# Performance work log

Measured on AMD Instinct MI355X. Metric: run time of the kernel, lower is better.

## Reference

```python
import jax, jax.numpy as jnp
import numpy as np

TOP_K = 2


def setup_inputs() -> dict:
    key = jax.random.key(0)
    k1, k2, k3, k4, k5 = jax.random.split(key, 5)
    B, S, H, F, E = 4, 2048, 1024, 4096, 8
    scale = 1.0 / np.sqrt(H)
    return {
        "hidden_states": jax.random.normal(k1, (B, S, H), dtype=jnp.float32),
        "gate_w": jax.random.normal(k2, (E, H), dtype=jnp.float32) * scale,
        "w1": jax.random.normal(k3, (E, F, H), dtype=jnp.float32) * scale,
        "w3": jax.random.normal(k4, (E, F, H), dtype=jnp.float32) * scale,
        "w2": jax.random.normal(k5, (E, H, F), dtype=jnp.float32) * (1.0 / np.sqrt(F)),
    }


def reference(hidden_states, gate_w, w1, w3, w2):
    B, S, H = hidden_states.shape
    E = gate_w.shape[0]
    x = hidden_states.reshape(-1, H)                    # [T, H], T = B*S

    router_logits = x @ gate_w.T                        # [T, E]
    probs = jax.nn.softmax(router_logits.astype(jnp.float32), axis=-1)
    top_w, top_i = jax.lax.top_k(probs, TOP_K)          # [T, k]
    top_w = top_w / jnp.sum(top_w, axis=-1, keepdims=True)
    top_w = top_w.astype(x.dtype)

    # combine weight of each expert for each token: [E, T]
    one_hot = jax.nn.one_hot(top_i, E, dtype=x.dtype)   # [T, k, E]
    comb = jnp.einsum("tke,tk->et", one_hot, top_w)

    # loop over experts via scan; tokens not routed to expert e have comb==0,
    # which matches the gather/FFN/scatter-combine of the original exactly.
    def body(acc, wts):
        w1e, w3e, w2e, ce = wts
        h = jax.nn.silu(x @ w1e.T) * (x @ w3e.T)        # [T, F]
        return acc + (h @ w2e.T) * ce[:, None], None

    out0 = jnp.zeros_like(x)
    out, _ = jax.lax.scan(body, out0, (w1, w3, w2, comb))
    return out.reshape(B, S, H), router_logits
```

## Files before the change

kernel.cpp:

```cpp
#include <hip/hip_runtime.h>
#include <hip/hip_bf16.h>

#define T_TOK 8192
#define HDIM  1024
#define FDIM  4096
#define NEXP  8
#define CVT_BLKS 2048
#define RT_MAX 24

typedef __attribute__((ext_vector_type(8))) short short8;
typedef __attribute__((ext_vector_type(4))) float f32x4;
typedef unsigned short u16;
typedef unsigned int   u32;

#define XB_OFF    0ull
#define W1B_OFF   (XB_OFF   + 16777216ull)
#define W3B_OFF   (W1B_OFF  + 67108864ull)
#define W2B_OFF   (W3B_OFF  + 67108864ull)
#define HBUF_OFF  (W2B_OFF  + 67108864ull)
#define CNT_OFF   (HBUF_OFF + 134217728ull)
#define TLIST_OFF (CNT_OFF  + 128ull)
#define WLIST_OFF (TLIST_OFF + 262144ull)
#define WS_NEED   (WLIST_OFF + 262144ull)

__device__ __forceinline__ u16 f2bf(float f) {
  u32 u = __float_as_uint(f);
  return (u16)((u + 0x7fffu + ((u >> 16) & 1u)) >> 16);
}
__device__ __forceinline__ float bf2f(u16 v) {
  return __uint_as_float((u32)v << 16);
}

__device__ __forceinline__ void gl_lds16(const void* g, void* l) {
  __builtin_amdgcn_global_load_lds(
      (const __attribute__((address_space(1))) void*)g,
      (__attribute__((address_space(3))) void*)l, 16, 0, 0);
}

__global__ __launch_bounds__(256) void prep_kernel(
    const float* __restrict__ x, const float* __restrict__ gw,
    const float* __restrict__ s0, const float* __restrict__ s1,
    u16* __restrict__ d0, u16* __restrict__ d1,
    float* __restrict__ logits, u16* __restrict__ xb,
    int* __restrict__ counts, int* __restrict__ tlist,
    float* __restrict__ wt1, float* __restrict__ wt2,
    int* __restrict__ slot1, int* __restrict__ slot2) {
  if (blockIdx.x < 8192) {
    const int n8 = NEXP * FDIM * HDIM / 8;
    const int total = 2 * n8;
    const int stride = 8192 * 256;
    for (int i = blockIdx.x * 256 + threadIdx.x; i < total; i += stride) {
      int seg = i >> 22;
      int j = i & (n8 - 1);
      const float* s = seg == 0 ? s0 : s1;
      u16* d = seg == 0 ? d0 : d1;
      float4 v0 = ((const float4*)s)[j * 2];
      float4 v1 = ((const float4*)s)[j * 2 + 1];
      uint4 o;
      o.x = (u32)f2bf(v0.x) | ((u32)f2bf(v0.y) << 16);
      o.y = (u32)f2bf(v0.z) | ((u32)f2bf(v0.w) << 16);
      o.z = (u32)f2bf(v1.x) | ((u32)f2bf(v1.y) << 16);
      o.w = (u32)f2bf(v1.z) | ((u32)f2bf(v1.w) << 16);
      ((uint4*)d)[j] = o;
    }
    return;
  }
  const int wid = threadIdx.x >> 6, lane = threadIdx.x & 63;
  const int t = (blockIdx.x - 8192) * 4 + wid;
  const float* xr = x + (size_t)t * HDIM + lane * 16;
  float4 xv[4];
#pragma unroll
  for (int q = 0; q < 4; ++q) xv[q] = ((const float4*)xr)[q];

  u32 pk[8];
#pragma unroll
  for (int q = 0; q < 4; ++q) {
    pk[q * 2 + 0] = (u32)f2bf(xv[q].x) | ((u32)f2bf(xv[q].y) << 16);
    pk[q * 2 + 1] = (u32)f2bf(xv[q].z) | ((u32)f2bf(xv[q].w) << 16);
  }
  u32* xbo = (u32*)(xb + (size_t)t * HDIM + lane * 16);
  ((uint4*)xbo)[0] = make_uint4(pk[0], pk[1], pk[2], pk[3]);
  ((uint4*)xbo)[1] = make_uint4(pk[4], pk[5], pk[6], pk[7]);

  float lg[NEXP];
#pragma unroll
  for (int e = 0; e < NEXP; ++e) {
    const float4* g = (const float4*)(gw + (size_t)e * HDIM + lane * 16);
    float s = 0.f;
#pragma unroll
    for (int q = 0; q < 4; ++q) {
      float4 gv = g[q];
      s += xv[q].x * gv.x + xv[q].y * gv.y + xv[q].z * gv.z + xv[q].w * gv.w;
    }
#pragma unroll
    for (int off = 32; off > 0; off >>= 1) s += __shfl_xor(s, off, 64);
    lg[e] = s;
  }
  if (lane == 0) {
    float* lo = logits + (size_t)t * NEXP;
#pragma unroll
    for (int e = 0; e < NEXP; ++e) lo[e] = lg[e];
    float v1 = -1e30f, v2 = -1e30f; int i1 = 0, i2 = 0;
#pragma unroll
    for (int e = 0; e < NEXP; ++e) {
      float le = lg[e];
      if (le > v1)      { v2 = v1; i2 = i1; v1 = le; i1 = e; }
      else if (le > v2) { v2 = le; i2 = e; }
    }
    float t2 = __expf(v2 - v1);
    float rs = 1.f / (1.f + t2);
    int p1 = atomicAdd(&counts[i1], 1);
    tlist[i1 * T_TOK + p1] = t;
    slot1[t] = (i1 << 16) | p1;  wt1[t] = rs;
    int p2 = atomicAdd(&counts[i2], 1);
    tlist[i2 * T_TOK + p2] = t;
    slot2[t] = (i2 << 16) | p2;  wt2[t] = t2 * rs;
  }
}

__global__ __launch_bounds__(256, 4) void ffn1_kernel(
    const u16* __restrict__ xb, const u16* __restrict__ w1b, const u16* __restrict__ w3b,
    u16* __restrict__ hbuf, const int* __restrict__ counts, const int* __restrict__ tlist,
    const float* __restrict__ w2src, u16* __restrict__ w2b) {
  if (blockIdx.x < CVT_BLKS) {
    const int n8 = NEXP * HDIM * FDIM / 8;
    const int stride = CVT_BLKS * 256;
    for (int j = blockIdx.x * 256 + threadIdx.x; j < n8; j += stride) {
      float4 v0 = ((const float4*)w2src)[j * 2];
      float4 v1 = ((const float4*)w2src)[j * 2 + 1];
      uint4 o;
      o.x = (u32)f2bf(v0.x) | ((u32)f2bf(v0.y) << 16);
      o.y = (u32)f2bf(v0.z) | ((u32)f2bf(v0.w) << 16);
      o.z = (u32)f2bf(v1.x) | ((u32)f2bf(v1.y) << 16);
      o.w = (u32)f2bf(v1.z) | ((u32)f2bf(v1.w) << 16);
      ((uint4*)w2b)[j] = o;
    }
    return;
  }
  const int bid = blockIdx.x - CVT_BLKS;
  const int e  = bid & 7;
  const int j  = bid >> 3;
  const int ct = j / RT_MAX;
  const int rt = j - ct * RT_MAX;
  const int Ne = counts[e];
  if (rt * 128 >= Ne) return;
  int hb = 0;
#pragma unroll
  for (int i = 0; i < NEXP; ++i) hb += (i < e) ? counts[i] : 0;

  __shared__ u16 LDS[16384];

  const int tid = threadIdx.x;
  const int wid = tid >> 6, lane = tid & 63;
  const int wr = wid >> 1, wc = wid & 1;
  const int lr = lane & 15, lhi = lane >> 4;

  size_t aoff[4];
#pragma unroll
  for (int q = 0; q < 4; ++q) {
    int idx = q * 256 + tid;
    int r = idx >> 3, c = idx & 7;
    int grow = rt * 128 + r;
    int gi = grow < Ne ? grow : Ne - 1;
    aoff[q] = (size_t)tlist[e * T_TOK + gi] * HDIM + (size_t)((c ^ (r & 7)) * 8);
  }
  size_t boff[2];
#pragma unroll
  for (int q = 0; q < 2; ++q) {
    int idx = q * 256 + tid;
    int r = idx >> 3, c = idx & 7;
    boff[q] = ((size_t)e * FDIM + ct * 64 + r) * HDIM + (size_t)((c ^ (r & 7)) * 8);
  }
  const int dW = wid * 64 * 8;

  f32x4 acc1[4][2] = {}, acc3[4][2] = {};

  for (int k0 = 0; k0 < HDIM; k0 += 64) {
    __syncthreads();
#pragma unroll
    for (int q = 0; q < 4; ++q)
      gl_lds16(xb + aoff[q] + k0, LDS + q * 2048 + dW);
#pragma unroll
    for (int q = 0; q < 2; ++q) {
      gl_lds16(w1b + boff[q] + k0, LDS + 8192 + q * 2048 + dW);
      gl_lds16(w3b + boff[q] + k0, LDS + 12288 + q * 2048 + dW);
    }
    __syncthreads();
#pragma unroll
    for (int kk = 0; kk < 2; ++kk) {
      const int chn = ((kk * 4 + lhi) ^ (lr & 7)) * 8;
      short8 af[4], b1f[2], b3f[2];
#pragma unroll
      for (int m = 0; m < 4; ++m)
        af[m] = *(const short8*)(LDS + (wr * 64 + m * 16 + lr) * 64 + chn);
#pragma unroll
      for (int n = 0; n < 2; ++n) {
        int ro = (wc * 32 + n * 16 + lr) * 64 + chn;
        b1f[n] = *(const short8*)(LDS + 8192 + ro);
        b3f[n] = *(const short8*)(LDS + 12288 + ro);
      }
#pragma unroll
      for (int m = 0; m < 4; ++m)
#pragma unroll
        for (int n = 0; n < 2; ++n) {
          acc1[m][n] = __builtin_amdgcn_mfma_f32_16x16x32_bf16(af[m], b1f[n], acc1[m][n], 0, 0, 0);
          acc3[m][n] = __builtin_amdgcn_mfma_f32_16x16x32_bf16(af[m], b3f[n], acc3[m][n], 0, 0, 0);
        }
    }
  }

  const int rbase = rt * 128 + wr * 64 + lhi * 4;
  const int cbase = ct * 64 + wc * 32 + lr;
#pragma unroll
  for (int m = 0; m < 4; ++m)
#pragma unroll
    for (int i = 0; i < 4; ++i) {
      int grow = rbase + m * 16 + i;
      if (grow < Ne) {
        size_t rowp = (size_t)(hb + grow) * FDIM + cbase;
#pragma unroll
        for (int n = 0; n < 2; ++n) {
          float a1 = acc1[m][n][i], a3 = acc3[m][n][i];
          hbuf[rowp + n * 16] = f2bf((a1 / (1.f + __expf(-a1))) * a3);
        }
      }
    }
}

__global__ __launch_bounds__(256, 4) void ffn2_kernel(
    const u16* __restrict__ hbuf, const u16* __restrict__ w2b,
    u16* __restrict__ ybuf, const int* __restrict__ counts) {
  const int bid = blockIdx.x;
  const int e  = bid & 7;
  const int j  = bid >> 3;
  const int ct = j / RT_MAX;
  const int rt = j - ct * RT_MAX;
  const int Ne = counts[e];
  if (rt * 128 >= Ne) return;
  int hb = 0;
#pragma unroll
  for (int i = 0; i < NEXP; ++i) hb += (i < e) ? counts[i] : 0;

  __shared__ u16 Alds[128 * 64];
  __shared__ u16 Blds[128 * 64];

  const int tid = threadIdx.x;
  const int wid = tid >> 6, lane = tid & 63;
  const int wr = wid >> 1, wc = wid & 1;
  const int lr = lane & 15, lhi = lane >> 4;

  size_t aoff[4], boff[4]; int ldso[4];
#pragma unroll
  for (int q = 0; q < 4; ++q) {
    int i = wid * 4 + q;
    int r = i * 8 + (lane >> 3);
    int sw = ((lane & 7) ^ (r & 7)) * 8;
    int grow = rt * 128 + r;
    int gi = grow < Ne ? grow : Ne - 1;
    aoff[q] = (size_t)(hb + gi) * FDIM + sw;
    int hr = ct * 128 + r;
    boff[q] = ((size_t)e * HDIM + hr) * FDIM + sw;
    ldso[q] = i * 512;
  }

  f32x4 acc[4][4] = {};

  for (int k0 = 0; k0 < FDIM; k0 += 64) {
    __syncthreads();
#pragma unroll
    for (int q = 0; q < 4; ++q) {
      gl_lds16(hbuf + aoff[q] + k0, Alds + ldso[q]);
      gl_lds16(w2b + boff[q] + k0, Blds + ldso[q]);
    }
    __syncthreads();
#pragma unroll
    for (int kk = 0; kk < 2; ++kk) {
      const int swo = ((kk * 4 + lhi) ^ (lr & 7)) * 8;
      short8 af[4], bf_[4];
#pragma unroll
      for (int m = 0; m < 4; ++m)
        af[m] = *(const short8*)(Alds + (wr * 64 + m * 16 + lr) * 64 + swo);
#pragma unroll
      for (int n = 0; n < 4; ++n)
        bf_[n] = *(const short8*)(Blds + (wc * 64 + n * 16 + lr) * 64 + swo);
#pragma unroll
      for (int m = 0; m < 4; ++m)
#pragma unroll
        for (int n = 0; n < 4; ++n)
          acc[m][n] = __builtin_amdgcn_mfma_f32_16x16x32_bf16(af[m], bf_[n], acc[m][n], 0, 0, 0);
    }
  }

  const int rb = rt * 128 + wr * 64 + lhi * 4;
  const int cb = ct * 128 + wc * 64 + lr;
#pragma unroll
  for (int m = 0; m < 4; ++m)
#pragma unroll
    for (int i = 0; i < 4; ++i) {
      int grow = rb + m * 16 + i;
      if (grow < Ne) {
        u16* yp = ybuf + (size_t)(hb + grow) * HDIM + cb;
#pragma unroll
        for (int n = 0; n < 4; ++n)
          yp[n * 16] = f2bf(acc[m][n][i]);
      }
    }
}

__global__ __launch_bounds__(256) void combine_kernel(
    const u16* __restrict__ ybuf, const int* __restrict__ slot1, const int* __restrict__ slot2,
    const float* __restrict__ wt1, const float* __restrict__ wt2,
    const int* __restrict__ counts, float* __restrict__ out) {
  int pre[NEXP + 1];
  pre[0] = 0;
#pragma unroll
  for (int i = 0; i < NEXP; ++i) pre[i + 1] = pre[i] + counts[i];
  int idx = blockIdx.x * 256 + threadIdx.x;
  int t = idx >> 7, c8 = (idx & 127) * 8;
  int s1 = slot1[t], s2 = slot2[t];
  float w1 = wt1[t], w2 = wt2[t];
  size_t r1 = (size_t)(pre[s1 >> 16] + (s1 & 0xFFFF)) * HDIM + c8;
  size_t r2 = (size_t)(pre[s2 >> 16] + (s2 & 0xFFFF)) * HDIM + c8;
  short8 y1 = *(const short8*)(ybuf + r1);
  short8 y2 = *(const short8*)(ybuf + r2);
  float* op = out + (size_t)t * HDIM + c8;
#pragma unroll
  for (int k = 0; k < 8; ++k)
    op[k] = w1 * bf2f((u16)y1[k]) + w2 * bf2f((u16)y2[k]);
}

extern "C" void kernel_launch(void* const* d_in, const int* in_sizes, int n_in,
                              void* d_out, int out_size, void* d_ws, size_t ws_size,
                              hipStream_t stream) {
  (void)in_sizes; (void)n_in; (void)out_size;
  if (ws_size < WS_NEED) return;

  const float* x  = (const float*)d_in[0];
  const float* gw = (const float*)d_in[1];
  const float* w1 = (const float*)d_in[2];
  const float* w3 = (const float*)d_in[3];
  const float* w2 = (const float*)d_in[4];
  float* out = (float*)d_out;
  float* logits = out + (size_t)T_TOK * HDIM;

  char* ws = (char*)d_ws;
  u16* xb    = (u16*)(ws + XB_OFF);
  u16* w1b   = (u16*)(ws + W1B_OFF);
  u16* w3b   = (u16*)(ws + W3B_OFF);
  u16* w2b   = (u16*)(ws + W2B_OFF);
  u16* hbuf  = (u16*)(ws + HBUF_OFF);
  u16* ybuf  = (u16*)(ws + W1B_OFF);
  int* counts = (int*)(ws + CNT_OFF);
  int* tlist  = (int*)(ws + TLIST_OFF);
  float* wt1  = (float*)(ws + WLIST_OFF);
  float* wt2  = wt1 + T_TOK;
  int* slot1  = (int*)(wt2 + T_TOK);
  int* slot2  = slot1 + T_TOK;

  hipMemsetAsync(counts, 0, NEXP * sizeof(int), stream);

  prep_kernel<<<8192 + 2048, 256, 0, stream>>>(x, gw, w1, w3, w1b, w3b,
                                               logits, xb, counts, tlist,
                                               wt1, wt2, slot1, slot2);
  ffn1_kernel<<<CVT_BLKS + NEXP * RT_MAX * 64, 256, 0, stream>>>(
      xb, w1b, w3b, hbuf, counts, tlist, w2, w2b);
  ffn2_kernel<<<NEXP * RT_MAX * 8, 256, 0, stream>>>(hbuf, w2b, ybuf, counts);
  combine_kernel<<<T_TOK * 128 / 256, 256, 0, stream>>>(ybuf, slot1, slot2, wt1, wt2, counts, out);
}
```

Baseline: 773.1 us.

## Fuse fp32-to-bf16 weight conversion into GEMM tile loads

```diff
diff --git a/kernel.cpp b/kernel.cpp
--- a/kernel.cpp
+++ b/kernel.cpp
@@ -5,7 +5,6 @@
 #define HDIM  1024
 #define FDIM  4096
 #define NEXP  8
-#define CVT_BLKS 2048
 #define RT_MAX 24
 
 typedef __attribute__((ext_vector_type(8))) short short8;
@@ -14,10 +13,8 @@
 typedef unsigned int   u32;
 
 #define XB_OFF    0ull
-#define W1B_OFF   (XB_OFF   + 16777216ull)
-#define W3B_OFF   (W1B_OFF  + 67108864ull)
-#define W2B_OFF   (W3B_OFF  + 67108864ull)
-#define HBUF_OFF  (W2B_OFF  + 67108864ull)
+#define YBUF_OFF  (XB_OFF   + 16777216ull)
+#define HBUF_OFF  (YBUF_OFF + 67108864ull)
 #define CNT_OFF   (HBUF_OFF + 134217728ull)
 #define TLIST_OFF (CNT_OFF  + 128ull)
 #define WLIST_OFF (TLIST_OFF + 262144ull)
@@ -30,6 +27,11 @@
 __device__ __forceinline__ float bf2f(u16 v) {
   return __uint_as_float((u32)v << 16);
 }
+__device__ __forceinline__ u32 cvt_pk(float lo, float hi) {
+  u32 r;
+  asm("v_cvt_pk_bf16_f32 %0, %1, %2" : "=v"(r) : "v"(lo), "v"(hi));
+  return r;
+}
 
 __device__ __forceinline__ void gl_lds16(const void* g, void* l) {
   __builtin_amdgcn_global_load_lds(
@@ -37,36 +39,14 @@
       (__attribute__((address_space(3))) void*)l, 16, 0, 0);
 }
 
-__global__ __launch_bounds__(256) void prep_kernel(
+__global__ __launch_bounds__(256) void router_kernel(
     const float* __restrict__ x, const float* __restrict__ gw,
-    const float* __restrict__ s0, const float* __restrict__ s1,
-    u16* __restrict__ d0, u16* __restrict__ d1,
     float* __restrict__ logits, u16* __restrict__ xb,
     int* __restrict__ counts, int* __restrict__ tlist,
     float* __restrict__ wt1, float* __restrict__ wt2,
     int* __restrict__ slot1, int* __restrict__ slot2) {
-  if (blockIdx.x < 8192) {
-    const int n8 = NEXP * FDIM * HDIM / 8;
-    const int total = 2 * n8;
-    const int stride = 8192 * 256;
-    for (int i = blockIdx.x * 256 + threadIdx.x; i < total; i += stride) {
-      int seg = i >> 22;
-      int j = i & (n8 - 1);
-      const float* s = seg == 0 ? s0 : s1;
-      u16* d = seg == 0 ? d0 : d1;
-      float4 v0 = ((const float4*)s)[j * 2];
-      float4 v1 = ((const float4*)s)[j * 2 + 1];
-      uint4 o;
-      o.x = (u32)f2bf(v0.x) | ((u32)f2bf(v0.y) << 16);
-      o.y = (u32)f2bf(v0.z) | ((u32)f2bf(v0.w) << 16);
-      o.z = (u32)f2bf(v1.x) | ((u32)f2bf(v1.y) << 16);
-      o.w = (u32)f2bf(v1.z) | ((u32)f2bf(v1.w) << 16);
-      ((uint4*)d)[j] = o;
-    }
-    return;
-  }
   const int wid = threadIdx.x >> 6, lane = threadIdx.x & 63;
-  const int t = (blockIdx.x - 8192) * 4 + wid;
+  const int t = blockIdx.x * 4 + wid;
   const float* xr = x + (size_t)t * HDIM + lane * 16;
   float4 xv[4];
 #pragma unroll
@@ -119,25 +99,9 @@
 }
 
 __global__ __launch_bounds__(256, 4) void ffn1_kernel(
-    const u16* __restrict__ xb, const u16* __restrict__ w1b, const u16* __restrict__ w3b,
-    u16* __restrict__ hbuf, const int* __restrict__ counts, const int* __restrict__ tlist,
-    const float* __restrict__ w2src, u16* __restrict__ w2b) {
-  if (blockIdx.x < CVT_BLKS) {
-    const int n8 = NEXP * HDIM * FDIM / 8;
-    const int stride = CVT_BLKS * 256;
-    for (int j = blockIdx.x * 256 + threadIdx.x; j < n8; j += stride) {
-      float4 v0 = ((const float4*)w2src)[j * 2];
-      float4 v1 = ((const float4*)w2src)[j * 2 + 1];
-      uint4 o;
-      o.x = (u32)f2bf(v0.x) | ((u32)f2bf(v0.y) << 16);
-      o.y = (u32)f2bf(v0.z) | ((u32)f2bf(v0.w) << 16);
-      o.z = (u32)f2bf(v1.x) | ((u32)f2bf(v1.y) << 16);
-      o.w = (u32)f2bf(v1.z) | ((u32)f2bf(v1.w) << 16);
-      ((uint4*)w2b)[j] = o;
-    }
-    return;
-  }
-  const int bid = blockIdx.x - CVT_BLKS;
+    const u16* __restrict__ xb, const float* __restrict__ w1, const float* __restrict__ w3,
+    u16* __restrict__ hbuf, const int* __restrict__ counts, const int* __restrict__ tlist) {
+  const int bid = blockIdx.x;
   const int e  = bid & 7;
   const int j  = bid >> 3;
   const int ct = j / RT_MAX;
@@ -164,26 +128,35 @@
     int gi = grow < Ne ? grow : Ne - 1;
     aoff[q] = (size_t)tlist[e * T_TOK + gi] * HDIM + (size_t)((c ^ (r & 7)) * 8);
   }
-  size_t boff[2];
-#pragma unroll
-  for (int q = 0; q < 2; ++q) {
-    int idx = q * 256 + tid;
-    int r = idx >> 3, c = idx & 7;
-    boff[q] = ((size_t)e * FDIM + ct * 64 + r) * HDIM + (size_t)((c ^ (r & 7)) * 8);
-  }
-  const int dW = wid * 64 * 8;
+  const int dW = wid * 512;
+
+  size_t boff[4]; int woff[4];
+#pragma unroll
+  for (int q = 0; q < 4; ++q) {
+    int s = q * 256 + tid;
+    int r = s >> 4, c32 = s & 15;
+    boff[q] = ((size_t)e * FDIM + ct * 64 + r) * HDIM + c32 * 4;
+    woff[q] = r * 64 + (((c32 >> 1) ^ (r & 7)) * 8) + (c32 & 1) * 4;
+  }
 
   f32x4 acc1[4][2] = {}, acc3[4][2] = {};
 
   for (int k0 = 0; k0 < HDIM; k0 += 64) {
+    float4 v1[4], v3[4];
+#pragma unroll
+    for (int q = 0; q < 4; ++q) v1[q] = *(const float4*)(w1 + boff[q] + k0);
+#pragma unroll
+    for (int q = 0; q < 4; ++q) v3[q] = *(const float4*)(w3 + boff[q] + k0);
     __syncthreads();
 #pragma unroll
     for (int q = 0; q < 4; ++q)
       gl_lds16(xb + aoff[q] + k0, LDS + q * 2048 + dW);
 #pragma unroll
-    for (int q = 0; q < 2; ++q) {
-      gl_lds16(w1b + boff[q] + k0, LDS + 8192 + q * 2048 + dW);
-      gl_lds16(w3b + boff[q] + k0, LDS + 12288 + q * 2048 + dW);
+    for (int q = 0; q < 4; ++q) {
+      uint2 p1; p1.x = cvt_pk(v1[q].x, v1[q].y); p1.y = cvt_pk(v1[q].z, v1[q].w);
+      *(uint2*)(LDS + 8192 + woff[q]) = p1;
+      uint2 p3; p3.x = cvt_pk(v3[q].x, v3[q].y); p3.y = cvt_pk(v3[q].z, v3[q].w);
+      *(uint2*)(LDS + 12288 + woff[q]) = p3;
     }
     __syncthreads();
 #pragma unroll
@@ -228,7 +201,7 @@
 }
 
 __global__ __launch_bounds__(256, 4) void ffn2_kernel(
-    const u16* __restrict__ hbuf, const u16* __restrict__ w2b,
+    const u16* __restrict__ hbuf, const float* __restrict__ w2,
     u16* __restrict__ ybuf, const int* __restrict__ counts) {
   const int bid = blockIdx.x;
   const int e  = bid & 7;
@@ -249,7 +222,7 @@
   const int wr = wid >> 1, wc = wid & 1;
   const int lr = lane & 15, lhi = lane >> 4;
 
-  size_t aoff[4], boff[4]; int ldso[4];
+  size_t aoff[4]; int ldso[4];
 #pragma unroll
   for (int q = 0; q < 4; ++q) {
     int i = wid * 4 + q;
@@ -258,19 +231,31 @@
     int grow = rt * 128 + r;
     int gi = grow < Ne ? grow : Ne - 1;
     aoff[q] = (size_t)(hb + gi) * FDIM + sw;
-    int hr = ct * 128 + r;
-    boff[q] = ((size_t)e * HDIM + hr) * FDIM + sw;
     ldso[q] = i * 512;
   }
+  size_t boff[8]; int woff[8];
+#pragma unroll
+  for (int q = 0; q < 8; ++q) {
+    int s = q * 256 + tid;
+    int r = s >> 4, c32 = s & 15;
+    boff[q] = ((size_t)e * HDIM + ct * 128 + r) * FDIM + c32 * 4;
+    woff[q] = r * 64 + (((c32 >> 1) ^ (r & 7)) * 8) + (c32 & 1) * 4;
+  }
 
   f32x4 acc[4][4] = {};
 
   for (int k0 = 0; k0 < FDIM; k0 += 64) {
+    float4 v[8];
+#pragma unroll
+    for (int q = 0; q < 8; ++q) v[q] = *(const float4*)(w2 + boff[q] + k0);
     __syncthreads();
 #pragma unroll
-    for (int q = 0; q < 4; ++q) {
+    for (int q = 0; q < 4; ++q)
       gl_lds16(hbuf + aoff[q] + k0, Alds + ldso[q]);
-      gl_lds16(w2b + boff[q] + k0, Blds + ldso[q]);
+#pragma unroll
+    for (int q = 0; q < 8; ++q) {
+      uint2 p; p.x = cvt_pk(v[q].x, v[q].y); p.y = cvt_pk(v[q].z, v[q].w);
+      *(uint2*)(Blds + woff[q]) = p;
     }
     __syncthreads();
 #pragma unroll
@@ -345,11 +330,8 @@
 
   char* ws = (char*)d_ws;
   u16* xb    = (u16*)(ws + XB_OFF);
-  u16* w1b   = (u16*)(ws + W1B_OFF);
-  u16* w3b   = (u16*)(ws + W3B_OFF);
-  u16* w2b   = (u16*)(ws + W2B_OFF);
+  u16* ybuf  = (u16*)(ws + YBUF_OFF);
   u16* hbuf  = (u16*)(ws + HBUF_OFF);
-  u16* ybuf  = (u16*)(ws + W1B_OFF);
   int* counts = (int*)(ws + CNT_OFF);
   int* tlist  = (int*)(ws + TLIST_OFF);
   float* wt1  = (float*)(ws + WLIST_OFF);
@@ -359,11 +341,9 @@
 
   hipMemsetAsync(counts, 0, NEXP * sizeof(int), stream);
 
-  prep_kernel<<<8192 + 2048, 256, 0, stream>>>(x, gw, w1, w3, w1b, w3b,
-                                               logits, xb, counts, tlist,
+  router_kernel<<<T_TOK / 4, 256, 0, stream>>>(x, gw, logits, xb, counts, tlist,
                                                wt1, wt2, slot1, slot2);
-  ffn1_kernel<<<CVT_BLKS + NEXP * RT_MAX * 64, 256, 0, stream>>>(
-      xb, w1b, w3b, hbuf, counts, tlist, w2, w2b);
-  ffn2_kernel<<<NEXP * RT_MAX * 8, 256, 0, stream>>>(hbuf, w2b, ybuf, counts);
+  ffn1_kernel<<<NEXP * RT_MAX * 64, 256, 0, stream>>>(xb, w1, w3, hbuf, counts, tlist);
+  ffn2_kernel<<<NEXP * RT_MAX * 8, 256, 0, stream>>>(hbuf, w2, ybuf, counts);
   combine_kernel<<<T_TOK * 128 / 256, 256, 0, stream>>>(ybuf, slot1, slot2, wt1, wt2, counts, out);
 }
```

Result: slower. 1.553 ms (+100.9%).
